# Optimization experiments

Measured on AMD Instinct MI355X. Metric: run time of the kernel, lower is better.

The kernel has to match this reference:

```python
import jax, jax.numpy as jnp
import numpy as np

N_ADDR = 400000
N_TX = 400000
E = 1500000
F_IN = 64
HID = 32
OUT = 2


def _sage(x_src, x_dst, ei, Wl, bl, Wr, n_dst):
    # SAGEConv: mean-aggregate source feats over incoming edges, then
    # out = lin_l(agg) + lin_r(x_dst). Nodes with no in-edges get agg=0.
    src, dst = ei[0], ei[1]
    msg = x_src[src]                                            # [E, F]
    s = jax.ops.segment_sum(msg, dst, num_segments=n_dst)       # [N_dst, F]
    cnt = jax.ops.segment_sum(jnp.ones((ei.shape[1], 1), x_src.dtype), dst,
                              num_segments=n_dst)               # [N_dst, 1]
    agg = s / jnp.maximum(cnt, 1.0)
    return agg @ Wl + bl + x_dst @ Wr


def setup_inputs() -> dict:
    key = jax.random.key(0)
    ks = jax.random.split(key, 24)
    d = {}
    d['x_addr'] = jax.random.normal(ks[0], (N_ADDR, F_IN), jnp.float32)
    d['x_tx'] = jax.random.normal(ks[1], (N_TX, F_IN), jnp.float32)
    d['ei_at'] = jax.random.randint(ks[2], (2, E), 0, N_ADDR)   # addr->tx (src idx < N_ADDR, dst idx < N_TX)
    d['ei_ta'] = jax.random.randint(ks[3], (2, E), 0, N_TX)     # tx->addr
    def w(k, i, o):
        return jax.random.normal(k, (i, o), jnp.float32) * (1.0 / np.sqrt(i))
    d['w1_tx_l'] = w(ks[4], F_IN, HID); d['b1_tx'] = jnp.zeros((HID,), jnp.float32)
    d['w1_tx_r'] = w(ks[5], F_IN, HID)
    d['w1_ad_l'] = w(ks[6], F_IN, HID); d['b1_ad'] = jnp.zeros((HID,), jnp.float32)
    d['w1_ad_r'] = w(ks[7], F_IN, HID)
    d['w2_tx_l'] = w(ks[8], HID, HID); d['b2_tx'] = jnp.zeros((HID,), jnp.float32)
    d['w2_tx_r'] = w(ks[9], HID, HID)
    d['w2_ad_l'] = w(ks[10], HID, HID); d['b2_ad'] = jnp.zeros((HID,), jnp.float32)
    d['w2_ad_r'] = w(ks[11], HID, HID)
    d['w3_tx_l'] = w(ks[12], HID, HID); d['b3_tx'] = jnp.zeros((HID,), jnp.float32)
    d['w3_tx_r'] = w(ks[13], HID, HID)
    d['w3_ad_l'] = w(ks[14], HID, HID); d['b3_ad'] = jnp.zeros((HID,), jnp.float32)
    d['w3_ad_r'] = w(ks[15], HID, HID)
    d['w_out'] = w(ks[16], HID, OUT); d['b_out'] = jnp.zeros((OUT,), jnp.float32)
    return d


def reference(x_addr, x_tx, ei_at, ei_ta,
              w1_tx_l, b1_tx, w1_tx_r, w1_ad_l, b1_ad, w1_ad_r,
              w2_tx_l, b2_tx, w2_tx_r, w2_ad_l, b2_ad, w2_ad_r,
              w3_tx_l, b3_tx, w3_tx_r, w3_ad_l, b3_ad, w3_ad_r,
              w_out, b_out):
    # Layer 1 (both node types updated simultaneously from previous x_dict)
    tx = jax.nn.relu(_sage(x_addr, x_tx, ei_at, w1_tx_l, b1_tx, w1_tx_r, N_TX))
    ad = jax.nn.relu(_sage(x_tx, x_addr, ei_ta, w1_ad_l, b1_ad, w1_ad_r, N_ADDR))
    # Layer 2
    tx2 = jax.nn.relu(_sage(ad, tx, ei_at, w2_tx_l, b2_tx, w2_tx_r, N_TX))
    ad2 = jax.nn.relu(_sage(tx, ad, ei_ta, w2_ad_l, b2_ad, w2_ad_r, N_ADDR))
    # Layer 3
    ad3 = jax.nn.relu(_sage(tx2, ad2, ei_ta, w3_ad_l, b3_ad, w3_ad_r, N_ADDR))
    # Final classifier on 'addr' nodes (dropout is identity at inference)
    return ad3 @ w_out + b_out
```

## Files before the change

kernel.cpp:

```cpp
#include <hip/hip_runtime.h>

#define NADDR 400000
#define NTX   400000
#define NEDGE 1500000
#define FIN   64
#define HID   32
#define NB    1563
#define LSTR  36
#define NND   400000
#define NHALF 200000

static inline int cdiv_host(long a, int b) { return (int)((a + b - 1) / b); }


__global__ void k_hist(const int* __restrict__ at_dst, const int* __restrict__ ta_dst,
                       int* __restrict__ bcnt , int GH) {
    __shared__ int h[NB];
    bool wh = blockIdx.x >= GH;
    int blk = blockIdx.x - (wh ? GH : 0);
    const int* dst = wh ? ta_dst : at_dst;
    for (int i = threadIdx.x; i < NB; i += 256) h[i] = 0;
    __syncthreads();
    for (long e = (long)blk * 256 + threadIdx.x; e < NEDGE; e += (long)GH * 256)
        atomicAdd(&h[dst[e] >> 8], 1);
    __syncthreads();
    int* g = bcnt + (wh ? NB : 0);
    for (int i = threadIdx.x; i < NB; i += 256) {
        int v = h[i];
        if (v) atomicAdd(&g[i], v);
    }
}

__global__ void k_scan_nb(const int* __restrict__ bcnt, int* __restrict__ bbase,
                          int* __restrict__ gcur) {
    __shared__ int sm[256];
    __shared__ int carry;
    int w = blockIdx.x;
    int t = threadIdx.x;
    if (t == 0) carry = 0;
    __syncthreads();
    for (int base = 0; base < NB; base += 256) {
        int i = base + t;
        int v = (i < NB) ? bcnt[w * NB + i] : 0;
        sm[t] = v;
        __syncthreads();
        for (int off = 1; off < 256; off <<= 1) {
            int x = (t >= off) ? sm[t - off] : 0;
            __syncthreads();
            sm[t] += x;
            __syncthreads();
        }
        int excl = sm[t] - v + carry;
        if (i < NB) { bbase[w * (NB + 1) + i] = excl; gcur[w * NB + i] = excl; }
        int tot = sm[255];
        __syncthreads();
        if (t == 0) carry += tot;
        __syncthreads();
    }
    if (t == 0) bbase[w * (NB + 1) + NB] = NEDGE;
}

__global__ void k_dist(const int* __restrict__ ei_at, const int* __restrict__ ei_ta,
                       int* __restrict__ gcur, unsigned* __restrict__ eb_at,
                       unsigned* __restrict__ eb_ta, int GD) {
    __shared__ int h[NB];
    __shared__ int bs[NB];
    bool wh = blockIdx.x >= GD;
    int blk = blockIdx.x - (wh ? GD : 0);
    const int* ei = wh ? ei_ta : ei_at;
    unsigned* eb = wh ? eb_ta : eb_at;
    for (int i = threadIdx.x; i < NB; i += 256) h[i] = 0;
    __syncthreads();
    long e0 = (long)blk * 256 + threadIdx.x;
    long stride = (long)GD * 256;
    for (long e = e0; e < NEDGE; e += stride)
        atomicAdd(&h[ei[NEDGE + e] >> 8], 1);
    __syncthreads();
    int* gc = gcur + (wh ? NB : 0);
    for (int i = threadIdx.x; i < NB; i += 256) {
        int c = h[i];
        bs[i] = c ? atomicAdd(&gc[i], c) : 0;
        h[i] = 0;
    }
    __syncthreads();
    for (long e = e0; e < NEDGE; e += stride) {
        int d = ei[NEDGE + e];
        int s = ei[e];
        int b = d >> 8;
        int r = atomicAdd(&h[b], 1);
        eb[bs[b] + r] = ((unsigned)s << 8) | (unsigned)(d & 255);
    }
}

__global__ void k_csrb(const unsigned* __restrict__ eb_at, const unsigned* __restrict__ eb_ta,
                       const int* __restrict__ bbase,
                       int* __restrict__ rp_tx, int* __restrict__ rp_ad,
                       int* __restrict__ col_at, int* __restrict__ col_ta) {
    __shared__ int deg[256];
    __shared__ int cur[256];
    __shared__ int sm[256];
    bool wh = blockIdx.x >= NB;
    int b = blockIdx.x - (wh ? NB : 0);
    const unsigned* eb = wh ? eb_ta : eb_at;
    int* rp  = wh ? rp_ad  : rp_tx;
    int* col = wh ? col_ta : col_at;
    const int* bb = bbase + (wh ? (NB + 1) : 0);
    int e0 = bb[b], e1 = bb[b + 1];
    int t = threadIdx.x;
    deg[t] = 0;
    __syncthreads();
    for (int e = e0 + t; e < e1; e += 256)
        atomicAdd(&deg[eb[e] & 255], 1);
    __syncthreads();
    int v = deg[t];
    sm[t] = v;
    __syncthreads();
    for (int off = 1; off < 256; off <<= 1) {
        int x = (t >= off) ? sm[t - off] : 0;
        __syncthreads();
        sm[t] += x;
        __syncthreads();
    }
    int excl = sm[t] - v;
    int node = b * 256 + t;
    if (node < NND) rp[node] = e0 + excl;
    cur[t] = e0 + excl;
    __syncthreads();
    for (int e = e0 + t; e < e1; e += 256) {
        unsigned p = eb[e];
        int idx = atomicAdd(&cur[p & 255], 1);
        col[idx] = (int)(p >> 8);
    }
    if (t == 0 && b == 0) rp[NND] = NEDGE;
}

__global__ __launch_bounds__(128)
void k_preS2(const float* __restrict__ x,
             const float* __restrict__ wa, float* __restrict__ outa,
             const float* __restrict__ wb, const float* __restrict__ bb,
             float* __restrict__ outb, int n) {
    __shared__ alignas(16) float xs[128 * LSTR];
    int t = threadIdx.x;
    long row0 = (long)blockIdx.x * 128;

    float aa[HID], ab[HID];
#pragma unroll
    for (int j = 0; j < HID; ++j) { aa[j] = 0.0f; ab[j] = bb[j]; }

    for (int kt = 0; kt < FIN / 32; ++kt) {
        if (kt) __syncthreads();
#pragma unroll
        for (int sub = 0; sub < 8; ++sub) {
            int f = sub * 128 + t;
            int r = f >> 3, k4 = f & 7;
            long gr = row0 + r;
            if (gr >= n) gr = n - 1;
            *(float4*)(&xs[r * LSTR + k4 * 4]) =
                *(const float4*)(x + gr * FIN + kt * 32 + k4 * 4);
        }
        __syncthreads();
        float xr[32];
#pragma unroll
        for (int q = 0; q < 8; ++q) {
            float4 v = *(const float4*)(&xs[t * LSTR + q * 4]);
            xr[q * 4] = v.x; xr[q * 4 + 1] = v.y; xr[q * 4 + 2] = v.z; xr[q * 4 + 3] = v.w;
        }
        const float* wka = wa + kt * 32 * HID;
        const float* wkb = wb + kt * 32 * HID;
#pragma unroll
        for (int k = 0; k < 32; ++k) {
            float xk = xr[k];
            const float* ra = wka + k * HID;
            const float* rb = wkb + k * HID;
#pragma unroll
            for (int j = 0; j < HID; ++j) {
                aa[j] = __builtin_fmaf(xk, ra[j], aa[j]);
                ab[j] = __builtin_fmaf(xk, rb[j], ab[j]);
            }
        }
    }

    __syncthreads();
#pragma unroll
    for (int j = 0; j < HID; j += 4)
        *(float4*)(&xs[t * LSTR + j]) = make_float4(aa[j], aa[j + 1], aa[j + 2], aa[j + 3]);
    __syncthreads();
#pragma unroll
    for (int sub = 0; sub < 8; ++sub) {
        int f = sub * 128 + t;
        int r = f >> 3, k4 = f & 7;
        long gr = row0 + r;
        if (gr < n)
            *(float4*)(outa + gr * HID + k4 * 4) = *(const float4*)(&xs[r * LSTR + k4 * 4]);
    }
    __syncthreads();
#pragma unroll
    for (int j = 0; j < HID; j += 4)
        *(float4*)(&xs[t * LSTR + j]) = make_float4(ab[j], ab[j + 1], ab[j + 2], ab[j + 3]);
    __syncthreads();
#pragma unroll
    for (int sub = 0; sub < 8; ++sub) {
        int f = sub * 128 + t;
        int r = f >> 3, k4 = f & 7;
        long gr = row0 + r;
        if (gr < n)
            *(float4*)(outb + gr * HID + k4 * 4) = *(const float4*)(&xs[r * LSTR + k4 * 4]);
    }
}

__global__ __launch_bounds__(256)
void k_preCMD(const float* __restrict__ xT,
              const float* __restrict__ wa, float* __restrict__ outa,
              const float* __restrict__ wb, const float* __restrict__ bb,
              float* __restrict__ outb) {
    int i = blockIdx.x * 256 + threadIdx.x;
    if (i >= NND) return;
    float aa[HID], ab[HID];
#pragma unroll
    for (int j = 0; j < HID; ++j) { aa[j] = 0.0f; ab[j] = bb[j]; }
#pragma unroll
    for (int k = 0; k < 32; ++k) {
        float f = xT[(size_t)k * NND + i];
        const float* ra = wa + k * HID;
        const float* rb = wb + k * HID;
#pragma unroll
        for (int j = 0; j < HID; ++j) {
            aa[j] = __builtin_fmaf(f, ra[j], aa[j]);
            ab[j] = __builtin_fmaf(f, rb[j], ab[j]);
        }
    }
    float* oa = outa + (size_t)i * HID;
    float* ob = outb + (size_t)i * HID;
#pragma unroll
    for (int j = 0; j < HID; j += 4) {
        *(float4*)(oa + j) = make_float4(aa[j], aa[j + 1], aa[j + 2], aa[j + 3]);
        *(float4*)(ob + j) = make_float4(ab[j], ab[j + 1], ab[j + 2], ab[j + 3]);
    }
}

__global__ __launch_bounds__(256, 2)
void k_preCM1(const float* __restrict__ xT, const float* __restrict__ w,
              const float* __restrict__ b, float* __restrict__ out) {
    int i = blockIdx.x * 256 + threadIdx.x;
    if (i >= NHALF) return;
    float a0[HID], a1[HID];
#pragma unroll
    for (int j = 0; j < HID; ++j) { float bv = b ? b[j] : 0.0f; a0[j] = bv; a1[j] = bv; }
#pragma unroll
    for (int k = 0; k < 32; ++k) {
        float f0 = xT[(size_t)k * NND + i];
        float f1 = xT[(size_t)k * NND + i + NHALF];
        const float* wr = w + k * HID;
#pragma unroll
        for (int j = 0; j < HID; ++j) {
            float wv = wr[j];
            a0[j] = __builtin_fmaf(f0, wv, a0[j]);
            a1[j] = __builtin_fmaf(f1, wv, a1[j]);
        }
    }
    float* o0 = out + (size_t)i * HID;
    float* o1 = out + (size_t)(i + NHALF) * HID;
#pragma unroll
    for (int j = 0; j < HID; j += 4) {
        *(float4*)(o0 + j) = make_float4(a0[j], a0[j + 1], a0[j + 2], a0[j + 3]);
        *(float4*)(o1 + j) = make_float4(a1[j], a1[j + 1], a1[j + 2], a1[j + 3]);
    }
}

template<bool CM, bool FINAL>
__global__ __launch_bounds__(256)
void k_agg(const int* __restrict__ rp, const int* __restrict__ col,
           const float* __restrict__ preL, const float* __restrict__ preR,
           float* __restrict__ y,
           const float* __restrict__ wo, const float* __restrict__ bo, int n) {
    int t = blockIdx.x * 256 + threadIdx.x;
    int g = t >> 3;
    int u = t & 7;
    if (g >= n) return;
    int p0 = rp[g], p1 = rp[g + 1];

    float ax = 0.0f, ay = 0.0f, az = 0.0f, aw = 0.0f;
    for (int k = p0; k < p1; k += 8) {
        int last = p1 - 1;
        int idx[8];
#pragma unroll
        for (int q = 0; q < 8; ++q) {
            int e = k + q;
            idx[q] = col[e < p1 ? e : last];
        }
        float4 v[8];
#pragma unroll
        for (int q = 0; q < 8; ++q)
            v[q] = *(const float4*)(preL + (size_t)idx[q] * HID + u * 4);
#pragma unroll
        for (int q = 0; q < 8; ++q) {
            if (k + q < p1) {
                ax += v[q].x; ay += v[q].y; az += v[q].z; aw += v[q].w;
            }
        }
    }
    float inv = 1.0f / fmaxf((float)(p1 - p0), 1.0f);
    float4 r = *(const float4*)(preR + (size_t)g * HID + u * 4);
    float4 h;
    h.x = fmaxf(__builtin_fmaf(ax, inv, r.x), 0.0f);
    h.y = fmaxf(__builtin_fmaf(ay, inv, r.y), 0.0f);
    h.z = fmaxf(__builtin_fmaf(az, inv, r.z), 0.0f);
    h.w = fmaxf(__builtin_fmaf(aw, inv, r.w), 0.0f);

    if (FINAL) {
        int j = u * 4;
        float o0 = h.x * wo[(j + 0) * 2 + 0] + h.y * wo[(j + 1) * 2 + 0]
                 + h.z * wo[(j + 2) * 2 + 0] + h.w * wo[(j + 3) * 2 + 0];
        float o1 = h.x * wo[(j + 0) * 2 + 1] + h.y * wo[(j + 1) * 2 + 1]
                 + h.z * wo[(j + 2) * 2 + 1] + h.w * wo[(j + 3) * 2 + 1];
#pragma unroll
        for (int m = 4; m >= 1; m >>= 1) {
            o0 += __shfl_xor(o0, m, 8);
            o1 += __shfl_xor(o1, m, 8);
        }
        if (u == 0) {
            y[(size_t)g * 2 + 0] = o0 + bo[0];
            y[(size_t)g * 2 + 1] = o1 + bo[1];
        }
    } else if (CM) {
        int c = u * 4;
        y[(size_t)(c + 0) * NND + g] = h.x;
        y[(size_t)(c + 1) * NND + g] = h.y;
        y[(size_t)(c + 2) * NND + g] = h.z;
        y[(size_t)(c + 3) * NND + g] = h.w;
    } else {
        *(float4*)(y + (size_t)g * HID + u * 4) = h;
    }
}


extern "C" void kernel_launch(void* const* d_in, const int* in_sizes, int n_in,
                              void* d_out, int out_size, void* d_ws, size_t ws_size,
                              hipStream_t stream) {
    const float* x_addr  = (const float*)d_in[0];
    const float* x_tx    = (const float*)d_in[1];
    const int*   ei_at   = (const int*)d_in[2];
    const int*   ei_ta   = (const int*)d_in[3];
    const float* w1_tx_l = (const float*)d_in[4];  const float* b1_tx = (const float*)d_in[5];
    const float* w1_tx_r = (const float*)d_in[6];
    const float* w1_ad_l = (const float*)d_in[7];  const float* b1_ad = (const float*)d_in[8];
    const float* w1_ad_r = (const float*)d_in[9];
    const float* w2_tx_l = (const float*)d_in[10]; const float* b2_tx = (const float*)d_in[11];
    const float* w2_tx_r = (const float*)d_in[12];
    const float* w2_ad_l = (const float*)d_in[13]; const float* b2_ad = (const float*)d_in[14];
    const float* w2_ad_r = (const float*)d_in[15];
    const float* w3_ad_l = (const float*)d_in[19]; const float* b3_ad = (const float*)d_in[20];
    const float* w3_ad_r = (const float*)d_in[21];
    const float* w_out   = (const float*)d_in[22]; const float* b_out = (const float*)d_in[23];
    float* out = (float*)d_out;

    char* base = (char*)d_ws;
    int* bcnt   = (int*)base;  base += (size_t)(2 * NB) * 4;
    int* bbase  = (int*)base;  base += (size_t)(2 * (NB + 1)) * 4;
    int* gcur   = (int*)base;  base += (size_t)(2 * NB) * 4;
    int* rp_tx  = (int*)base;  base += (size_t)(NND + 1) * 4;
    int* rp_ad  = (int*)base;  base += (size_t)(NND + 1) * 4;
    int* col_at = (int*)base;  base += (size_t)NEDGE * 4;
    int* col_ta = (int*)base;  base += (size_t)NEDGE * 4;
    base = (char*)(((size_t)base + 255) & ~(size_t)255);
    const size_t SLOT = (size_t)NND * HID;
    float* E = (float*)base;
    unsigned* eb_at = (unsigned*)base;
    unsigned* eb_ta = eb_at + (size_t)NEDGE;
    float* A = E + SLOT;
    float* B = A + SLOT;
    float* C = B + SLOT;
    float* D = C + SLOT;

    dim3 blk(256);
    dim3 blk128(128);
    int gS  = cdiv_host(NND, 128);
    int gD  = cdiv_host(NND, 256);
    int gCM = cdiv_host(NHALF, 256);
    int gG  = cdiv_host((long)NND * 8, 256);
    const int GH = 96, GD = 192;

    hipMemsetAsync(bcnt, 0, (size_t)(2 * NB) * 4, stream);
    k_hist<<<2 * GH, blk, 0, stream>>>(ei_at + NEDGE, ei_ta + NEDGE, bcnt, GH);
    k_scan_nb<<<2, blk, 0, stream>>>(bcnt, bbase, gcur);
    k_dist<<<2 * GD, blk, 0, stream>>>(ei_at, ei_ta, gcur, eb_at, eb_ta, GD);
    k_csrb<<<2 * NB, blk, 0, stream>>>(eb_at, eb_ta, bbase, rp_tx, rp_ad, col_at, col_ta);

    k_preS2<<<gS, blk128, 0, stream>>>(x_addr, w1_tx_l, A, w1_ad_r, b1_ad, B, NADDR);
    k_preS2<<<gS, blk128, 0, stream>>>(x_tx, w1_ad_l, C, w1_tx_r, b1_tx, D, NTX);
    k_agg<true, false><<<gG, blk, 0, stream>>>(rp_tx, col_at, A, D, E, nullptr, nullptr, NTX);
    k_agg<true, false><<<gG, blk, 0, stream>>>(rp_ad, col_ta, C, B, A, nullptr, nullptr, NADDR);

    k_preCMD<<<gD, blk, 0, stream>>>(A, w2_tx_l, B, w2_ad_r, b2_ad, C);
    k_preCMD<<<gD, blk, 0, stream>>>(E, w2_ad_l, D, w2_tx_r, b2_tx, A);
    k_agg<true, false><<<gG, blk, 0, stream>>>(rp_tx, col_at, B, A, E, nullptr, nullptr, NTX);
    k_agg<true, false><<<gG, blk, 0, stream>>>(rp_ad, col_ta, D, C, A, nullptr, nullptr, NADDR);

    k_preCM1<<<gCM, blk, 0, stream>>>(E, w3_ad_l, nullptr, B);
    k_preCM1<<<gCM, blk, 0, stream>>>(A, w3_ad_r, b3_ad, C);
    k_agg<false, true><<<gG, blk, 0, stream>>>(rp_ad, col_ta, B, C, out, w_out, b_out, NADDR);
}
```

Before: 718.9 us.

## Fuse next-layer linear transforms into the aggregation kernel epilogue

Replaces the separate column-major projection kernels (k_preCMD, k_preCM1) and the aggregation kernel with a single k_aggE. It gathers neighbours, applies mean, residual and ReLU, stages the hidden rows in shared memory, and then applies the next layer's left/right weight matrices (or the final classifier) per row. This removes the write and re-read of the hidden activations between layers and cuts several kernel launches. In exchange, each block now walks 256 destination rows in 8 serial passes before the epilogue, which may reduce gather parallelism. The per-thread 32×32 mat-vec also adds register pressure.

After: 673.9 us, median of 2. 1.07x faster.

```diff
diff --git a/kernel.cpp b/kernel.cpp
--- a/kernel.cpp
+++ b/kernel.cpp
@@ -7,8 +7,8 @@
 #define HID   32
 #define NB    1563
 #define LSTR  36
+#define HSTR  36
 #define NND   400000
-#define NHALF 200000
 
 static inline int cdiv_host(long a, int b) { return (int)((a + b - 1) / b); }
 
@@ -208,128 +208,108 @@
     }
 }
 
+template<int EP>
 __global__ __launch_bounds__(256)
-void k_preCMD(const float* __restrict__ xT,
-              const float* __restrict__ wa, float* __restrict__ outa,
-              const float* __restrict__ wb, const float* __restrict__ bb,
-              float* __restrict__ outb) {
-    int i = blockIdx.x * 256 + threadIdx.x;
-    if (i >= NND) return;
-    float aa[HID], ab[HID];
-#pragma unroll
-    for (int j = 0; j < HID; ++j) { aa[j] = 0.0f; ab[j] = bb[j]; }
-#pragma unroll
-    for (int k = 0; k < 32; ++k) {
-        float f = xT[(size_t)k * NND + i];
-        const float* ra = wa + k * HID;
-        const float* rb = wb + k * HID;
-#pragma unroll
-        for (int j = 0; j < HID; ++j) {
-            aa[j] = __builtin_fmaf(f, ra[j], aa[j]);
-            ab[j] = __builtin_fmaf(f, rb[j], ab[j]);
-        }
-    }
-    float* oa = outa + (size_t)i * HID;
-    float* ob = outb + (size_t)i * HID;
-#pragma unroll
-    for (int j = 0; j < HID; j += 4) {
-        *(float4*)(oa + j) = make_float4(aa[j], aa[j + 1], aa[j + 2], aa[j + 3]);
-        *(float4*)(ob + j) = make_float4(ab[j], ab[j + 1], ab[j + 2], ab[j + 3]);
-    }
-}
-
-__global__ __launch_bounds__(256, 2)
-void k_preCM1(const float* __restrict__ xT, const float* __restrict__ w,
-              const float* __restrict__ b, float* __restrict__ out) {
-    int i = blockIdx.x * 256 + threadIdx.x;
-    if (i >= NHALF) return;
-    float a0[HID], a1[HID];
-#pragma unroll
-    for (int j = 0; j < HID; ++j) { float bv = b ? b[j] : 0.0f; a0[j] = bv; a1[j] = bv; }
-#pragma unroll
-    for (int k = 0; k < 32; ++k) {
-        float f0 = xT[(size_t)k * NND + i];
-        float f1 = xT[(size_t)k * NND + i + NHALF];
-        const float* wr = w + k * HID;
-#pragma unroll
-        for (int j = 0; j < HID; ++j) {
-            float wv = wr[j];
-            a0[j] = __builtin_fmaf(f0, wv, a0[j]);
-            a1[j] = __builtin_fmaf(f1, wv, a1[j]);
-        }
-    }
-    float* o0 = out + (size_t)i * HID;
-    float* o1 = out + (size_t)(i + NHALF) * HID;
-#pragma unroll
-    for (int j = 0; j < HID; j += 4) {
-        *(float4*)(o0 + j) = make_float4(a0[j], a0[j + 1], a0[j + 2], a0[j + 3]);
-        *(float4*)(o1 + j) = make_float4(a1[j], a1[j + 1], a1[j + 2], a1[j + 3]);
-    }
-}
-
-template<bool CM, bool FINAL>
-__global__ __launch_bounds__(256)
-void k_agg(const int* __restrict__ rp, const int* __restrict__ col,
-           const float* __restrict__ preL, const float* __restrict__ preR,
-           float* __restrict__ y,
-           const float* __restrict__ wo, const float* __restrict__ bo, int n) {
-    int t = blockIdx.x * 256 + threadIdx.x;
-    int g = t >> 3;
+void k_aggE(const int* __restrict__ rp, const int* __restrict__ col,
+            const float* __restrict__ preL, const float* preR,
+            const float* __restrict__ wA, const float* __restrict__ bA, float* outA,
+            const float* __restrict__ wB, const float* __restrict__ bB, float* outB,
+            int n) {
+    __shared__ alignas(16) float hh[256 * HSTR];
+    int t = threadIdx.x;
+    long row0 = (long)blockIdx.x * 256;
     int u = t & 7;
-    if (g >= n) return;
-    int p0 = rp[g], p1 = rp[g + 1];
-
-    float ax = 0.0f, ay = 0.0f, az = 0.0f, aw = 0.0f;
-    for (int k = p0; k < p1; k += 8) {
-        int last = p1 - 1;
-        int idx[8];
-#pragma unroll
-        for (int q = 0; q < 8; ++q) {
-            int e = k + q;
-            idx[q] = col[e < p1 ? e : last];
-        }
-        float4 v[8];
-#pragma unroll
-        for (int q = 0; q < 8; ++q)
-            v[q] = *(const float4*)(preL + (size_t)idx[q] * HID + u * 4);
-#pragma unroll
-        for (int q = 0; q < 8; ++q) {
-            if (k + q < p1) {
-                ax += v[q].x; ay += v[q].y; az += v[q].z; aw += v[q].w;
+    int lnb = t >> 3;
+
+    for (int bi = 0; bi < 8; ++bi) {
+        int ln = bi * 32 + lnb;
+        long g = row0 + ln;
+        if (g < n) {
+            int p0 = rp[g], p1 = rp[g + 1];
+            float ax = 0.0f, ay = 0.0f, az = 0.0f, aw = 0.0f;
+            for (int k = p0; k < p1; k += 8) {
+                int last = p1 - 1;
+                int idx[8];
+#pragma unroll
+                for (int q = 0; q < 8; ++q) {
+                    int e = k + q;
+                    idx[q] = col[e < p1 ? e : last];
+                }
+                float4 v[8];
+#pragma unroll
+                for (int q = 0; q < 8; ++q)
+                    v[q] = *(const float4*)(preL + (size_t)idx[q] * HID + u * 4);
+#pragma unroll
+                for (int q = 0; q < 8; ++q) {
+                    if (k + q < p1) {
+                        ax += v[q].x; ay += v[q].y; az += v[q].z; aw += v[q].w;
+                    }
+                }
             }
-        }
-    }
-    float inv = 1.0f / fmaxf((float)(p1 - p0), 1.0f);
-    float4 r = *(const float4*)(preR + (size_t)g * HID + u * 4);
-    float4 h;
-    h.x = fmaxf(__builtin_fmaf(ax, inv, r.x), 0.0f);
-    h.y = fmaxf(__builtin_fmaf(ay, inv, r.y), 0.0f);
-    h.z = fmaxf(__builtin_fmaf(az, inv, r.z), 0.0f);
-    h.w = fmaxf(__builtin_fmaf(aw, inv, r.w), 0.0f);
-
-    if (FINAL) {
-        int j = u * 4;
-        float o0 = h.x * wo[(j + 0) * 2 + 0] + h.y * wo[(j + 1) * 2 + 0]
-                 + h.z * wo[(j + 2) * 2 + 0] + h.w * wo[(j + 3) * 2 + 0];
-        float o1 = h.x * wo[(j + 0) * 2 + 1] + h.y * wo[(j + 1) * 2 + 1]
-                 + h.z * wo[(j + 2) * 2 + 1] + h.w * wo[(j + 3) * 2 + 1];
-#pragma unroll
-        for (int m = 4; m >= 1; m >>= 1) {
-            o0 += __shfl_xor(o0, m, 8);
-            o1 += __shfl_xor(o1, m, 8);
-        }
-        if (u == 0) {
-            y[(size_t)g * 2 + 0] = o0 + bo[0];
-            y[(size_t)g * 2 + 1] = o1 + bo[1];
-        }
-    } else if (CM) {
-        int c = u * 4;
-        y[(size_t)(c + 0) * NND + g] = h.x;
-        y[(size_t)(c + 1) * NND + g] = h.y;
-        y[(size_t)(c + 2) * NND + g] = h.z;
-        y[(size_t)(c + 3) * NND + g] = h.w;
-    } else {
-        *(float4*)(y + (size_t)g * HID + u * 4) = h;
+            float inv = 1.0f / fmaxf((float)(p1 - p0), 1.0f);
+            float4 r = *(const float4*)(preR + (size_t)g * HID + u * 4);
+            float* hp = &hh[ln * HSTR + u * 4];
+            hp[0] = fmaxf(__builtin_fmaf(ax, inv, r.x), 0.0f);
+            hp[1] = fmaxf(__builtin_fmaf(ay, inv, r.y), 0.0f);
+            hp[2] = fmaxf(__builtin_fmaf(az, inv, r.z), 0.0f);
+            hp[3] = fmaxf(__builtin_fmaf(aw, inv, r.w), 0.0f);
+        }
+    }
+    __syncthreads();
+
+    long gd = row0 + t;
+    if (gd >= n) return;
+    float rrow[32];
+#pragma unroll
+    for (int q = 0; q < 8; ++q) {
+        float4 v = *(const float4*)(&hh[t * HSTR + q * 4]);
+        rrow[q * 4] = v.x; rrow[q * 4 + 1] = v.y;
+        rrow[q * 4 + 2] = v.z; rrow[q * 4 + 3] = v.w;
+    }
+
+    if (EP == 2) {
+        float o0 = bA[0], o1 = bA[1];
+#pragma unroll
+        for (int k = 0; k < HID; ++k) {
+            o0 = __builtin_fmaf(rrow[k], wA[k * 2 + 0], o0);
+            o1 = __builtin_fmaf(rrow[k], wA[k * 2 + 1], o1);
+        }
+        outA[gd * 2 + 0] = o0;
+        outA[gd * 2 + 1] = o1;
+        return;
+    }
+
+    {
+        float acc[HID];
+#pragma unroll
+        for (int j = 0; j < HID; ++j) acc[j] = bA ? bA[j] : 0.0f;
+#pragma unroll
+        for (int k = 0; k < HID; ++k) {
+            float rk = rrow[k];
+            const float* wr = wA + k * HID;
+#pragma unroll
+            for (int j = 0; j < HID; ++j) acc[j] = __builtin_fmaf(rk, wr[j], acc[j]);
+        }
+        float* o = outA + (size_t)gd * HID;
+#pragma unroll
+        for (int j = 0; j < HID; j += 4)
+            *(float4*)(o + j) = make_float4(acc[j], acc[j + 1], acc[j + 2], acc[j + 3]);
+    }
+    if (EP == 0) {
+        float acc[HID];
+#pragma unroll
+        for (int j = 0; j < HID; ++j) acc[j] = bB[j];
+#pragma unroll
+        for (int k = 0; k < HID; ++k) {
+            float rk = rrow[k];
+            const float* wr = wB + k * HID;
+#pragma unroll
+            for (int j = 0; j < HID; ++j) acc[j] = __builtin_fmaf(rk, wr[j], acc[j]);
+        }
+        float* o = outB + (size_t)gd * HID;
+#pragma unroll
+        for (int j = 0; j < HID; j += 4)
+            *(float4*)(o + j) = make_float4(acc[j], acc[j + 1], acc[j + 2], acc[j + 3]);
     }
 }
 
@@ -364,20 +344,18 @@
     int* col_ta = (int*)base;  base += (size_t)NEDGE * 4;
     base = (char*)(((size_t)base + 255) & ~(size_t)255);
     const size_t SLOT = (size_t)NND * HID;
-    float* E = (float*)base;
+    float* SE = (float*)base;
     unsigned* eb_at = (unsigned*)base;
     unsigned* eb_ta = eb_at + (size_t)NEDGE;
-    float* A = E + SLOT;
-    float* B = A + SLOT;
-    float* C = B + SLOT;
-    float* D = C + SLOT;
+    float* SA = SE + SLOT;
+    float* SB = SA + SLOT;
+    float* SC = SB + SLOT;
+    float* SD = SC + SLOT;
 
     dim3 blk(256);
     dim3 blk128(128);
-    int gS  = cdiv_host(NND, 128);
-    int gD  = cdiv_host(NND, 256);
-    int gCM = cdiv_host(NHALF, 256);
-    int gG  = cdiv_host((long)NND * 8, 256);
+    int gS = cdiv_host(NND, 128);
+    int gB = cdiv_host(NND, 256);
     const int GH = 96, GD = 192;
 
     hipMemsetAsync(bcnt, 0, (size_t)(2 * NB) * 4, stream);
@@ -386,17 +364,24 @@
     k_dist<<<2 * GD, blk, 0, stream>>>(ei_at, ei_ta, gcur, eb_at, eb_ta, GD);
     k_csrb<<<2 * NB, blk, 0, stream>>>(eb_at, eb_ta, bbase, rp_tx, rp_ad, col_at, col_ta);
 
-    k_preS2<<<gS, blk128, 0, stream>>>(x_addr, w1_tx_l, A, w1_ad_r, b1_ad, B, NADDR);
-    k_preS2<<<gS, blk128, 0, stream>>>(x_tx, w1_ad_l, C, w1_tx_r, b1_tx, D, NTX);
-    k_agg<true, false><<<gG, blk, 0, stream>>>(rp_tx, col_at, A, D, E, nullptr, nullptr, NTX);
-    k_agg<true, false><<<gG, blk, 0, stream>>>(rp_ad, col_ta, C, B, A, nullptr, nullptr, NADDR);
-
-    k_preCMD<<<gD, blk, 0, stream>>>(A, w2_tx_l, B, w2_ad_r, b2_ad, C);
-    k_preCMD<<<gD, blk, 0, stream>>>(E, w2_ad_l, D, w2_tx_r, b2_tx, A);
-    k_agg<true, false><<<gG, blk, 0, stream>>>(rp_tx, col_at, B, A, E, nullptr, nullptr, NTX);
-    k_agg<true, false><<<gG, blk, 0, stream>>>(rp_ad, col_ta, D, C, A, nullptr, nullptr, NADDR);
-
-    k_preCM1<<<gCM, blk, 0, stream>>>(E, w3_ad_l, nullptr, B);
-    k_preCM1<<<gCM, blk, 0, stream>>>(A, w3_ad_r, b3_ad, C);
-    k_agg<false, true><<<gG, blk, 0, stream>>>(rp_ad, col_ta, B, C, out, w_out, b_out, NADDR);
-}
+    k_preS2<<<gS, blk128, 0, stream>>>(x_addr, w1_tx_l, SA, w1_ad_r, b1_ad, SB, NADDR);
+    k_preS2<<<gS, blk128, 0, stream>>>(x_tx, w1_ad_l, SC, w1_tx_r, b1_tx, SD, NTX);
+
+    k_aggE<0><<<gB, blk, 0, stream>>>(rp_tx, col_at, SA, SD,
+                                      w2_ad_l, nullptr, SE,
+                                      w2_tx_r, b2_tx, SD, NTX);
+    k_aggE<0><<<gB, blk, 0, stream>>>(rp_ad, col_ta, SC, SB,
+                                      w2_tx_l, nullptr, SA,
+                                      w2_ad_r, b2_ad, SB, NADDR);
+
+    k_aggE<1><<<gB, blk, 0, stream>>>(rp_tx, col_at, SA, SD,
+                                      w3_ad_l, nullptr, SC,
+                                      nullptr, nullptr, nullptr, NTX);
+    k_aggE<1><<<gB, blk, 0, stream>>>(rp_ad, col_ta, SE, SB,
+                                      w3_ad_r, b3_ad, SB,
+                                      nullptr, nullptr, nullptr, NADDR);
+
+    k_aggE<2><<<gB, blk, 0, stream>>>(rp_ad, col_ta, SC, SB,
+                                      w_out, b_out, out,
+                                      nullptr, nullptr, nullptr, NADDR);
+}
```
